# Optimization experiments

Measured on AMD Instinct MI355X. Metric: run time of the kernel, lower is better.

Reference implementation:

```python
import jax, jax.numpy as jnp
import numpy as np

TGT_LEN = 1024
MEM_LEN = 1024
SAME_LENGTH = True
D_MODEL = 2048
BATCH = 4


def _make_ft_real(tgt_len: int, mem_len: int, same_length: bool) -> jnp.ndarray:
    """Build the banded Fourier mixing matrix. Since the module's input x is real
    and only .real of the output is returned, Re(FT @ x) == Re(FT) @ x, so we
    precompute only the real part (this also matches the kernel-headroom note:
    the imaginary output is never used)."""
    qlen = tgt_len
    klen = tgt_len + mem_len
    flen = klen - qlen + 1
    m = np.outer(np.arange(qlen), np.arange(flen))
    ft = np.exp(2j * np.pi * m / flen) / np.sqrt(flen)  # [qlen, flen] complex
    ft = np.pad(ft, ((0, 0), (klen - flen, 0)))          # left-pad to [qlen, klen]
    for i in range(qlen):  # setup-time numpy loop over fixed qlen rows (not traced)
        ft[i] = np.roll(ft[i], -(qlen - i - 1))
    ft = np.tril(ft, klen - qlen)
    if same_length:
        ft = np.triu(ft, 0)
    return jnp.asarray(ft.real.astype(np.float32))


_FT_REAL = _make_ft_real(TGT_LEN, MEM_LEN, SAME_LENGTH)  # [tgt_len, tgt_len+mem_len]


def setup_inputs() -> dict:
    key = jax.random.key(0)
    k1, k2 = jax.random.split(key)
    klen = TGT_LEN + MEM_LEN
    x = jax.random.normal(k1, (BATCH, klen, D_MODEL), dtype=jnp.float32)
    p = jax.random.normal(k2, (BATCH, klen, D_MODEL), dtype=jnp.float32)
    return {"x": x, "p": p, "qlen": TGT_LEN, "add_position": 1}


def reference(x, p, qlen, add_position):
    # Dropout is identity in eval mode (deterministic reference).
    if add_position:
        x = x + p
    klen = x.shape[1]
    ft = _FT_REAL[-qlen:, -klen:]                    # [qlen, klen]
    scale = np.float32(1.0 / np.sqrt(klen))
    # Banded token-mixing matmul; real part only (x is real).
    out = jnp.einsum("lm,bmd->bld", ft, x) * scale   # [B, qlen, D]
    return out
```

## Files before the change

kernel.cpp:

```cpp
#include <hip/hip_runtime.h>
#include <hip/hip_bf16.h>
#include <cstdint>

#define QLEN   1024
#define KLEN   2048
#define DMODEL 2048
#define BATCH  4
#define FLEN   (KLEN - QLEN + 1)

typedef __bf16 bf16x8 __attribute__((ext_vector_type(8)));
typedef float  f32x4  __attribute__((ext_vector_type(4)));

__device__ __align__(16) __bf16 g_ft[(size_t)QLEN * KLEN];
__device__ __align__(16) __bf16 g_yt[(size_t)BATCH * DMODEL * KLEN];

typedef __attribute__((address_space(1))) void gvoid;
typedef __attribute__((address_space(3))) void svoid;

__device__ __forceinline__ void async_load16(const void* g, void* lds) {
  gvoid* gp = (gvoid*)(uintptr_t)g;
  svoid* sp = (svoid*)(uint32_t)(uintptr_t)lds;
  __builtin_amdgcn_global_load_lds(gp, sp, 16, 0, 0);
}

#define YT_UNITS (BATCH * (KLEN / 8) * (DMODEL / 64))
#define FT_UNITS ((QLEN * KLEN) / 512)

__global__ __launch_bounds__(256) void prep_kernel(const float* __restrict__ x,
                                                   const float* __restrict__ p,
                                                   const int* __restrict__ addp) {
  const int lane  = threadIdx.x & 63;
  const int gw    = (blockIdx.x * 256 + threadIdx.x) >> 6;
  const int nw    = gridDim.x * 4;
  const int doadd = *addp;

  for (int u = gw; u < YT_UNITS + FT_UNITS; u += nw) {
    if (u < YT_UNITS) {
      const int b  = u >> 13;
      const int r5 = u & 8191;
      const int mt = r5 >> 5;
      const int db = r5 & 31;
      const int d  = db * 64 + lane;
      const float* xp = x + ((size_t)b * KLEN + mt * 8) * DMODEL + d;
      float v[8];
#pragma unroll
      for (int i = 0; i < 8; ++i) v[i] = xp[(size_t)i * DMODEL];
      if (doadd) {
        const float* pp = p + ((size_t)b * KLEN + mt * 8) * DMODEL + d;
#pragma unroll
        for (int i = 0; i < 8; ++i) v[i] += pp[(size_t)i * DMODEL];
      }
      bf16x8 o;
#pragma unroll
      for (int i = 0; i < 8; ++i) o[i] = (__bf16)v[i];
      *(bf16x8*)(g_yt + ((size_t)b * (KLEN / 8) * DMODEL + (size_t)mt * DMODEL + d) * 8) = o;
    } else {
      const int uu = (u - YT_UNITS) * 64 + lane;
      const int l  = uu >> 8;
      const int m0 = (uu & 255) * 8;
      const int j0 = m0 - l;
      bf16x8 o = {};
      if (j0 + 7 >= 0 && j0 < FLEN) {
        const float w     = 6.283185307179586f / (float)FLEN;
        const float scale = 1.0f / sqrtf((float)FLEN * (float)KLEN);
#pragma unroll
        for (int i = 0; i < 8; ++i) {
          const int j = j0 + i;
          float vv = 0.0f;
          if (j >= 0 && j < FLEN) {
            const int rr = (l * j) % FLEN;
            vv = cosf((float)rr * w) * scale;
          }
          o[i] = (__bf16)vv;
        }
      }
      *(bf16x8*)(g_ft + (size_t)uu * 8) = o;
    }
  }
}

#define BM 128
#define BN 128
#define BK 64

__global__ __launch_bounds__(256) void gemm_kernel(float* __restrict__ out) {
  __shared__ __align__(16) __bf16 As[BM * BK];
  __shared__ __align__(16) __bf16 Bs[BN * BK];
  const int bn = blockIdx.x, bm = blockIdx.y, b = blockIdx.z;
  const int l0 = bm * BM, d0 = bn * BN;
  const int tid  = threadIdx.x;
  const int lane = tid & 63;
  const int wave = tid >> 6;
  const int wr = wave >> 1, wc = wave & 1;
  const int col = lane & 15, quad = lane >> 4;

  f32x4 acc[4][4] = {};

  const int t0 = l0 >> 6;
  const int t1 = (l0 + BM - 1 + FLEN - 1) >> 6;
  const __bf16* ftp = g_ft;
  const __bf16* ytp = g_yt + (size_t)b * DMODEL * KLEN;

  for (int t = t0; t <= t1; ++t) {
    const int k0 = t * BK;
#pragma unroll
    for (int s = 0; s < 4; ++s) {
      const int cb  = wave * 256 + s * 64;
      const int lc  = cb + lane;
      const int row = lc >> 3;
      const int gc8 = (lc & 7) ^ (row & 7);
      async_load16(ftp + (size_t)(l0 + row) * KLEN + k0 + gc8 * 8, As + cb * 8);
    }
#pragma unroll
    for (int s = 0; s < 4; ++s) {
      const int idx = wave * 256 + s * 64 + lane;
      const int c   = idx >> 7;
      const int dd  = idx & 127;
      async_load16(ytp + ((size_t)(t * 8 + c) * DMODEL + (d0 + dd)) * 8, Bs + (size_t)idx * 8);
    }
    __syncthreads();

#pragma unroll
    for (int kk = 0; kk < 2; ++kk) {
      bf16x8 af[4], bq[4];
      const int c8 = kk * 4 + quad;
#pragma unroll
      for (int ti = 0; ti < 4; ++ti) {
        const int r = wr * 64 + ti * 16 + col;
        af[ti] = *(const bf16x8*)(As + (size_t)((r << 3) + (c8 ^ (r & 7))) * 8);
      }
#pragma unroll
      for (int tj = 0; tj < 4; ++tj) {
        const int r = wc * 64 + tj * 16 + col;
        bq[tj] = *(const bf16x8*)(Bs + (size_t)((c8 << 7) + r) * 8);
      }
#pragma unroll
      for (int ti = 0; ti < 4; ++ti)
#pragma unroll
        for (int tj = 0; tj < 4; ++tj)
          acc[ti][tj] = __builtin_amdgcn_mfma_f32_16x16x32_bf16(af[ti], bq[tj], acc[ti][tj], 0, 0, 0);
    }
    __syncthreads();
  }

#pragma unroll
  for (int ti = 0; ti < 4; ++ti) {
    const int l = l0 + wr * 64 + ti * 16 + quad * 4;
#pragma unroll
    for (int tj = 0; tj < 4; ++tj) {
      const int d = d0 + wc * 64 + tj * 16 + col;
      float* op = out + (size_t)b * QLEN * DMODEL + (size_t)l * DMODEL + d;
#pragma unroll
      for (int r2 = 0; r2 < 4; ++r2) op[(size_t)r2 * DMODEL] = acc[ti][tj][r2];
    }
  }
}

extern "C" void kernel_launch(void* const* d_in, const int* in_sizes, int n_in,
                              void* d_out, int out_size, void* d_ws, size_t ws_size,
                              hipStream_t stream) {
  const float* x   = (const float*)d_in[0];
  const float* p   = (const float*)d_in[1];
  const int* addp  = (const int*)d_in[3];
  float* out = (float*)d_out;

  prep_kernel<<<dim3(2048), dim3(256), 0, stream>>>(x, p, addp);
  gemm_kernel<<<dim3(DMODEL / BN, QLEN / BM, BATCH), dim3(256), 0, stream>>>(out);
}
```

Before: 195.5 us.

## Fuse x+p add and bf16 conversion into GEMM B-tile loading

```diff
diff --git a/kernel.cpp b/kernel.cpp
--- a/kernel.cpp
+++ b/kernel.cpp
@@ -12,7 +12,6 @@
 typedef float  f32x4  __attribute__((ext_vector_type(4)));
 
 __device__ __align__(16) __bf16 g_ft[(size_t)QLEN * KLEN];
-__device__ __align__(16) __bf16 g_yt[(size_t)BATCH * DMODEL * KLEN];
 
 typedef __attribute__((address_space(1))) void gvoid;
 typedef __attribute__((address_space(3))) void svoid;
@@ -23,67 +22,41 @@
   __builtin_amdgcn_global_load_lds(gp, sp, 16, 0, 0);
 }
 
-#define YT_UNITS (BATCH * (KLEN / 8) * (DMODEL / 64))
-#define FT_UNITS ((QLEN * KLEN) / 512)
-
-__global__ __launch_bounds__(256) void prep_kernel(const float* __restrict__ x,
-                                                   const float* __restrict__ p,
-                                                   const int* __restrict__ addp) {
-  const int lane  = threadIdx.x & 63;
-  const int gw    = (blockIdx.x * 256 + threadIdx.x) >> 6;
-  const int nw    = gridDim.x * 4;
-  const int doadd = *addp;
-
-  for (int u = gw; u < YT_UNITS + FT_UNITS; u += nw) {
-    if (u < YT_UNITS) {
-      const int b  = u >> 13;
-      const int r5 = u & 8191;
-      const int mt = r5 >> 5;
-      const int db = r5 & 31;
-      const int d  = db * 64 + lane;
-      const float* xp = x + ((size_t)b * KLEN + mt * 8) * DMODEL + d;
-      float v[8];
+__global__ __launch_bounds__(256) void prep_ft_kernel(__bf16* __restrict__ ftp) {
+  __bf16* ft = ftp ? ftp : g_ft;
+  const int uu = blockIdx.x * 256 + threadIdx.x;
+  const int l  = uu >> 8;
+  const int m0 = (uu & 255) * 8;
+  const int j0 = m0 - l;
+  bf16x8 o = {};
+  if (j0 + 7 >= 0 && j0 < FLEN) {
+    const float w     = 6.283185307179586f / (float)FLEN;
+    const float scale = 1.0f / sqrtf((float)FLEN * (float)KLEN);
 #pragma unroll
-      for (int i = 0; i < 8; ++i) v[i] = xp[(size_t)i * DMODEL];
-      if (doadd) {
-        const float* pp = p + ((size_t)b * KLEN + mt * 8) * DMODEL + d;
-#pragma unroll
-        for (int i = 0; i < 8; ++i) v[i] += pp[(size_t)i * DMODEL];
+    for (int i = 0; i < 8; ++i) {
+      const int j = j0 + i;
+      float vv = 0.0f;
+      if (j >= 0 && j < FLEN) {
+        const int rr = (l * j) % FLEN;
+        vv = cosf((float)rr * w) * scale;
       }
-      bf16x8 o;
-#pragma unroll
-      for (int i = 0; i < 8; ++i) o[i] = (__bf16)v[i];
-      *(bf16x8*)(g_yt + ((size_t)b * (KLEN / 8) * DMODEL + (size_t)mt * DMODEL + d) * 8) = o;
-    } else {
-      const int uu = (u - YT_UNITS) * 64 + lane;
-      const int l  = uu >> 8;
-      const int m0 = (uu & 255) * 8;
-      const int j0 = m0 - l;
-      bf16x8 o = {};
-      if (j0 + 7 >= 0 && j0 < FLEN) {
-        const float w     = 6.283185307179586f / (float)FLEN;
-        const float scale = 1.0f / sqrtf((float)FLEN * (float)KLEN);
-#pragma unroll
-        for (int i = 0; i < 8; ++i) {
-          const int j = j0 + i;
-          float vv = 0.0f;
-          if (j >= 0 && j < FLEN) {
-            const int rr = (l * j) % FLEN;
-            vv = cosf((float)rr * w) * scale;
-          }
-          o[i] = (__bf16)vv;
-        }
-      }
-      *(bf16x8*)(g_ft + (size_t)uu * 8) = o;
+      o[i] = (__bf16)vv;
     }
   }
+  *(bf16x8*)(ft + (size_t)uu * 8) = o;
 }
 
 #define BM 128
 #define BN 128
 #define BK 64
 
-__global__ __launch_bounds__(256) void gemm_kernel(float* __restrict__ out) {
+__device__ __forceinline__ int swz7(int i) { return i ^ ((i >> 3) & 7); }
+
+__global__ __launch_bounds__(256) void gemm_kernel(float* __restrict__ out,
+                                                   const __bf16* __restrict__ ftq,
+                                                   const float* __restrict__ x,
+                                                   const float* __restrict__ p,
+                                                   const int* __restrict__ addp) {
   __shared__ __align__(16) __bf16 As[BM * BK];
   __shared__ __align__(16) __bf16 Bs[BN * BK];
   const int bn = blockIdx.x, bm = blockIdx.y, b = blockIdx.z;
@@ -93,13 +66,24 @@
   const int wave = tid >> 6;
   const int wr = wave >> 1, wc = wave & 1;
   const int col = lane & 15, quad = lane >> 4;
+  const float addf = (*addp) ? 1.0f : 0.0f;
 
   f32x4 acc[4][4] = {};
 
+  const int cB = tid >> 5;
+  const int dg = tid & 31;
+  int wsw[4];
+#pragma unroll
+  for (int j = 0; j < 4; ++j) wsw[j] = cB * 128 + swz7(dg * 4 + j);
+  int rsw[4];
+#pragma unroll
+  for (int tj = 0; tj < 4; ++tj) rsw[tj] = swz7(wc * 64 + tj * 16 + col);
+
   const int t0 = l0 >> 6;
   const int t1 = (l0 + BM - 1 + FLEN - 1) >> 6;
-  const __bf16* ftp = g_ft;
-  const __bf16* ytp = g_yt + (size_t)b * DMODEL * KLEN;
+  const __bf16* ftp = ftq ? ftq : g_ft;
+  const float* xb0 = x + (size_t)b * KLEN * DMODEL + d0 + dg * 4;
+  const float* pb0 = p + (size_t)b * KLEN * DMODEL + d0 + dg * 4;
 
   for (int t = t0; t <= t1; ++t) {
     const int k0 = t * BK;
@@ -111,12 +95,21 @@
       const int gc8 = (lc & 7) ^ (row & 7);
       async_load16(ftp + (size_t)(l0 + row) * KLEN + k0 + gc8 * 8, As + cb * 8);
     }
+    {
+      const float* xb = xb0 + (size_t)(k0 + cB * 8) * DMODEL;
+      const float* pb = pb0 + (size_t)(k0 + cB * 8) * DMODEL;
+      f32x4 vx[8], vp[8];
 #pragma unroll
-    for (int s = 0; s < 4; ++s) {
-      const int idx = wave * 256 + s * 64 + lane;
-      const int c   = idx >> 7;
-      const int dd  = idx & 127;
-      async_load16(ytp + ((size_t)(t * 8 + c) * DMODEL + (d0 + dd)) * 8, Bs + (size_t)idx * 8);
+      for (int i = 0; i < 8; ++i) vx[i] = *(const f32x4*)(xb + (size_t)i * DMODEL);
+#pragma unroll
+      for (int i = 0; i < 8; ++i) vp[i] = *(const f32x4*)(pb + (size_t)i * DMODEL);
+#pragma unroll
+      for (int j = 0; j < 4; ++j) {
+        bf16x8 o;
+#pragma unroll
+        for (int i = 0; i < 8; ++i) o[i] = (__bf16)(vx[i][j] + addf * vp[i][j]);
+        *(bf16x8*)(Bs + (size_t)wsw[j] * 8) = o;
+      }
     }
     __syncthreads();
 
@@ -131,8 +124,7 @@
       }
 #pragma unroll
       for (int tj = 0; tj < 4; ++tj) {
-        const int r = wc * 64 + tj * 16 + col;
-        bq[tj] = *(const bf16x8*)(Bs + (size_t)((c8 << 7) + r) * 8);
+        bq[tj] = *(const bf16x8*)(Bs + (size_t)((c8 << 7) + rsw[tj]) * 8);
       }
 #pragma unroll
       for (int ti = 0; ti < 4; ++ti)
@@ -164,6 +156,9 @@
   const int* addp  = (const int*)d_in[3];
   float* out = (float*)d_out;
 
-  prep_kernel<<<dim3(2048), dim3(256), 0, stream>>>(x, p, addp);
-  gemm_kernel<<<dim3(DMODEL / BN, QLEN / BM, BATCH), dim3(256), 0, stream>>>(out);
+  const size_t FT_BYTES = (size_t)QLEN * KLEN * sizeof(__bf16);
+  __bf16* ft = (d_ws && ws_size >= FT_BYTES) ? (__bf16*)d_ws : nullptr;
+
+  prep_ft_kernel<<<dim3((QLEN * KLEN / 8) / 256), dim3(256), 0, stream>>>(ft);
+  gemm_kernel<<<dim3(DMODEL / BN, QLEN / BM, BATCH), dim3(256), 0, stream>>>(out, ft, x, p, addp);
 }
```

Result: slower. 221.9 us (+13.5%).
